# Performance work log

Hardware: AMD Instinct MI355X
Metric: run time of the kernel (lower is better)

Reference implementation:

```python
import jax, jax.numpy as jnp
import numpy as np

B = 128        # batch (images/texts)
N = 2048       # other texts per image
F_IMG = 1024   # raw image feature dim (abstracted encoder input)
F_TXT = 512    # raw text feature dim
D = 512        # embedding dim (num_features=512 in BasicNet)
TOPK = B - 1   # default topK = batch - 1


def setup_inputs() -> dict:
    key = jax.random.key(0)
    ks = jax.random.split(key, 6)
    return {
        "input_images": jax.random.normal(ks[0], (B, F_IMG), jnp.float32),
        "input_texts": jax.random.normal(ks[1], (B, F_TXT), jnp.float32),
        "other_texts": jax.random.normal(ks[2], (B, N, F_TXT), jnp.float32),
        "W_img": jax.random.normal(ks[3], (F_IMG, D), jnp.float32) / np.float32(np.sqrt(F_IMG)),
        "W_txt": jax.random.normal(ks[4], (F_TXT, D), jnp.float32) / np.float32(np.sqrt(F_TXT)),
        "logit_scale": jnp.asarray(np.log(1.0 / 0.07), jnp.float32),
    }


def reference(input_images, input_texts, other_texts, W_img, W_txt, logit_scale):
    K = TOPK
    # encoders abstracted as linear projections to D=512
    img = input_images @ W_img                                   # [B, D]
    img = img / jnp.linalg.norm(img, axis=1, keepdims=True)      # L2-normalize images
    txt = input_texts @ W_txt                                    # [B, D]
    txt = txt / jnp.linalg.norm(txt, axis=1, keepdims=True)      # row-wise norm == norm after concat
    oth = jnp.einsum('bnf,fd->bnd', other_texts, W_txt)          # [B, N, D]
    oth = oth / jnp.linalg.norm(oth, axis=2, keepdims=True)

    scale = jnp.exp(logit_scale)
    logit_in = scale * jnp.sum(img * txt, axis=1)                # [B] image_i . text_i
    logit_oth = scale * jnp.einsum('bd,bnd->bn', img, oth)       # [B, N]

    # descending sort + take top-K (lax.top_k returns sorted descending)
    topk_vals, _ = jax.lax.top_k(logit_oth, K)                   # [B, K]

    # indices = sorted(range(K) + [min(i, K-1)]): duplicate element p=min(i,K-1)
    rows = jnp.arange(B)
    cols = jnp.arange(K + 1)[None, :]                            # [1, K+1]
    p = jnp.minimum(rows, K - 1)[:, None]                        # [B, 1]
    gidx = jnp.where(cols <= p, cols, cols - 1)                  # [B, K+1]
    gathered = jnp.take_along_axis(topk_vals, gidx, axis=1)      # [B, K+1]

    # overwrite column i of row i with the positive (input text) logit
    out = jnp.where(cols == rows[:, None], logit_in[:, None], gathered)
    return out
```

## Files before the change

### kernel.cpp

```cpp
#include <hip/hip_runtime.h>
#include <hip/hip_bf16.h>
#include <math.h>

#define B_SZ 128
#define N_OTH 2048
#define F_IMG 1024
#define F_TXT 512
#define D_EMB 512
#define TOT (B_SZ * N_OTH)

typedef __attribute__((ext_vector_type(8))) short short8;
typedef __attribute__((ext_vector_type(16))) float f32x16;

static __device__ __forceinline__ ushort f2bf(float f) {
    __hip_bfloat16 h = __float2bfloat16(f);
    return *reinterpret_cast<ushort*>(&h);
}

static __device__ __forceinline__ void glds16(const float* g, float* l) {
    __builtin_amdgcn_global_load_lds((const __attribute__((address_space(1))) void*)g,
                                     (__attribute__((address_space(3))) void*)l, 16, 0, 0);
}

__global__ __launch_bounds__(512) void k_prep(const float* __restrict__ in_img,
                                              const float* __restrict__ in_txt,
                                              const float* __restrict__ W_img,
                                              const float* __restrict__ W_txt,
                                              const float* __restrict__ p_ls,
                                              float* __restrict__ img,
                                              float* __restrict__ logit_in,
                                              ushort* __restrict__ wf) {
    if (blockIdx.x >= B_SZ) {
        const int g = (blockIdx.x - B_SZ) * 512 + threadIdx.x;
        const int l = g & 63;
        const int frag = g >> 6;
        const int kstep = frag >> 4;
        const int ct = frag & 15;
        const int col = ct * 32 + (l & 31);
        const int kb = kstep * 16 + (l >> 5) * 8;
        short8 o;
#pragma unroll
        for (int j = 0; j < 8; ++j) o[j] = (short)f2bf(W_txt[(kb + j) * D_EMB + col]);
        *(short8*)(wf + (size_t)g * 8) = o;
        return;
    }
    const int b = blockIdx.x;
    const int d = threadIdx.x;
    __shared__ float row[F_IMG];
    __shared__ float wsum[8];
    __shared__ float s_rn;
    const int lane = d & 63, wv = d >> 6;

    for (int i = d; i < F_IMG; i += 512) row[i] = in_img[b * F_IMG + i];
    __syncthreads();
    float acc = 0.f;
#pragma unroll 8
    for (int f = 0; f < F_IMG; ++f) acc = fmaf(row[f], W_img[f * D_EMB + d], acc);
    float sq = acc * acc;
#pragma unroll
    for (int off = 32; off > 0; off >>= 1) sq += __shfl_down(sq, off);
    if (lane == 0) wsum[wv] = sq;
    __syncthreads();
    if (d == 0) {
        float s = 0.f;
        for (int w = 0; w < 8; ++w) s += wsum[w];
        s_rn = 1.0f / sqrtf(s);
    }
    __syncthreads();
    const float iv = acc * s_rn;
    img[b * D_EMB + d] = iv;

    __syncthreads();
    row[d] = in_txt[b * F_TXT + d];
    __syncthreads();
    float tacc = 0.f;
#pragma unroll 8
    for (int f = 0; f < F_TXT; ++f) tacc = fmaf(row[f], W_txt[f * D_EMB + d], tacc);
    float tsq = tacc * tacc;
#pragma unroll
    for (int off = 32; off > 0; off >>= 1) tsq += __shfl_down(tsq, off);
    __syncthreads();
    if (lane == 0) wsum[wv] = tsq;
    __syncthreads();
    if (d == 0) {
        float s = 0.f;
        for (int w = 0; w < 8; ++w) s += wsum[w];
        s_rn = 1.0f / sqrtf(s);
    }
    __syncthreads();
    float pd = (tacc * s_rn) * iv;
#pragma unroll
    for (int off = 32; off > 0; off >>= 1) pd += __shfl_down(pd, off);
    __syncthreads();
    if (lane == 0) wsum[wv] = pd;
    __syncthreads();
    if (d == 0) {
        float s = 0.f;
        for (int w = 0; w < 8; ++w) s += wsum[w];
        logit_in[b] = expf(p_ls[0]) * s;
    }
}

__global__ __launch_bounds__(256, 3) void k_gemm(const float* __restrict__ oth,
                                                 const ushort* __restrict__ wf,
                                                 const float* __restrict__ img,
                                                 float* __restrict__ numA,
                                                 float* __restrict__ denA) {
    __shared__ float sA[3][64 * 64];
    __shared__ float redN[4][64];
    __shared__ float redD[4][64];
    const int tid = threadIdx.x;
    const int l = tid & 63;
    const int wv = tid >> 6;
    const int strip = blockIdx.x >> 1;
    const int h = blockIdx.x & 1;
    const int b = strip >> 5;
    const size_t row0 = (size_t)strip * 64;

    const float* gA[4];
#pragma unroll
    for (int j = 0; j < 4; ++j) {
        const int row = wv * 16 + j * 4 + (l >> 4);
        const int gcol = (l & 15) ^ (row & 7);
        gA[j] = oth + (row0 + row) * F_TXT + gcol * 4;
    }

    const ushort* wbase = wf + ((size_t)(h * 8 + wv * 2) * 64 + l) * 8;

    f32x16 acc[2][2];
#pragma unroll
    for (int m = 0; m < 2; ++m)
#pragma unroll
        for (int n = 0; n < 2; ++n)
#pragma unroll
            for (int r = 0; r < 16; ++r) acc[m][n][r] = 0.f;

#pragma unroll
    for (int j = 0; j < 4; ++j) glds16(gA[j] + 0 * 64, &sA[0][(wv * 16 + j * 4) * 64]);
#pragma unroll
    for (int j = 0; j < 4; ++j) glds16(gA[j] + 1 * 64, &sA[1][(wv * 16 + j * 4) * 64]);
    __builtin_amdgcn_sched_barrier(0);
    asm volatile("s_waitcnt vmcnt(4)" ::: "memory");
    __builtin_amdgcn_sched_barrier(0);
    __builtin_amdgcn_s_barrier();
    __builtin_amdgcn_sched_barrier(0);

#pragma unroll
    for (int t = 0; t < 8; ++t) {
        const int cur = t % 3;
        short8 bfr[4][2];
#pragma unroll
        for (int ks = 0; ks < 4; ++ks)
#pragma unroll
            for (int n = 0; n < 2; ++n)
                bfr[ks][n] = *(const short8*)(wbase + (size_t)((t * 4 + ks) * 16 + n) * 512);
        __builtin_amdgcn_sched_barrier(0);
        if (t < 6) {
#pragma unroll
            for (int j = 0; j < 4; ++j)
                glds16(gA[j] + (t + 2) * 64, &sA[(t + 2) % 3][(wv * 16 + j * 4) * 64]);
        }
        __builtin_amdgcn_sched_barrier(0);
        __builtin_amdgcn_s_setprio(1);
#pragma unroll
        for (int ks = 0; ks < 4; ++ks) {
            short8 af[2];
#pragma unroll
            for (int m = 0; m < 2; ++m) {
                const int r = m * 32 + (l & 31);
                const int g0 = ks * 4 + (l >> 5) * 2;
                const float4 fa = *(const float4*)&sA[cur][r * 64 + ((g0 ^ (r & 7)) << 2)];
                const float4 fb = *(const float4*)&sA[cur][r * 64 + (((g0 + 1) ^ (r & 7)) << 2)];
                short8 v;
                v[0] = (short)f2bf(fa.x); v[1] = (short)f2bf(fa.y);
                v[2] = (short)f2bf(fa.z); v[3] = (short)f2bf(fa.w);
                v[4] = (short)f2bf(fb.x); v[5] = (short)f2bf(fb.y);
                v[6] = (short)f2bf(fb.z); v[7] = (short)f2bf(fb.w);
                af[m] = v;
            }
#pragma unroll
            for (int m = 0; m < 2; ++m)
#pragma unroll
                for (int n = 0; n < 2; ++n)
                    acc[m][n] = __builtin_amdgcn_mfma_f32_32x32x16_bf16(af[m], bfr[ks][n], acc[m][n], 0, 0, 0);
        }
        __builtin_amdgcn_s_setprio(0);
        if (t < 7) {
            asm volatile("s_waitcnt lgkmcnt(0)" ::: "memory");
            __builtin_amdgcn_sched_barrier(0);
            __builtin_amdgcn_s_barrier();
            __builtin_amdgcn_sched_barrier(0);
        }
    }

    float ic[2];
#pragma unroll
    for (int n = 0; n < 2; ++n)
        ic[n] = img[b * D_EMB + h * 256 + wv * 64 + n * 32 + (l & 31)];
#pragma unroll
    for (int m = 0; m < 2; ++m) {
#pragma unroll
        for (int rg = 0; rg < 16; ++rg) {
            const float p = acc[m][0][rg];
            const float q = acc[m][1][rg];
            float tn = p * ic[0] + q * ic[1];
            float td = p * p + q * q;
#pragma unroll
            for (int off = 1; off <= 16; off <<= 1) {
                tn += __shfl_xor(tn, off);
                td += __shfl_xor(td, off);
            }
            if ((l & 31) == 0) {
                const int r = m * 32 + (rg & 3) + 8 * (rg >> 2) + 4 * (l >> 5);
                redN[wv][r] = tn;
                redD[wv][r] = td;
            }
        }
    }
    __syncthreads();
    if (tid < 64) {
        float tn = 0.f, td = 0.f;
#pragma unroll
        for (int w = 0; w < 4; ++w) { tn += redN[w][tid]; td += redD[w][tid]; }
        numA[(size_t)h * TOT + row0 + tid] = tn;
        denA[(size_t)h * TOT + row0 + tid] = td;
    }
}

__global__ __launch_bounds__(512) void k_topk(const float* __restrict__ numA,
                                              const float* __restrict__ denA,
                                              const float* __restrict__ logit_in,
                                              const float* __restrict__ p_ls,
                                              float* __restrict__ out) {
    const int b = blockIdx.x;
    const int tid = threadIdx.x;
    const float scale = expf(p_ls[0]);
    __shared__ float a[N_OTH];
    for (int i = tid; i < N_OTH; i += 512) {
        const size_t idx = (size_t)b * N_OTH + i;
        const float nu = numA[idx] + numA[TOT + idx];
        const float de = denA[idx] + denA[TOT + idx];
        a[i] = scale * nu / sqrtf(de);
    }
    __syncthreads();
    for (unsigned k = 2; k <= N_OTH; k <<= 1) {
        for (unsigned j = k >> 1; j > 0; j >>= 1) {
#pragma unroll
            for (int s = 0; s < N_OTH / 512; ++s) {
                const unsigned i = tid + s * 512u;
                const unsigned ixj = i ^ j;
                if (ixj > i) {
                    const bool asc = ((i & k) == 0);
                    const float x = a[i], y = a[ixj];
                    if ((x > y) == asc) { a[i] = y; a[ixj] = x; }
                }
            }
            __syncthreads();
        }
    }
    if (tid < 128) {
        const int j = tid;
        float v;
        if (j == b) {
            v = logit_in[b];
        } else {
            const int m = j - (j > b ? 1 : 0);
            v = a[N_OTH - 1 - m];
        }
        out[b * 128 + j] = v;
    }
}

extern "C" void kernel_launch(void* const* d_in, const int* in_sizes, int n_in,
                              void* d_out, int out_size, void* d_ws, size_t ws_size,
                              hipStream_t stream) {
    const float* in_img = (const float*)d_in[0];
    const float* in_txt = (const float*)d_in[1];
    const float* oth    = (const float*)d_in[2];
    const float* W_img  = (const float*)d_in[3];
    const float* W_txt  = (const float*)d_in[4];
    const float* p_ls   = (const float*)d_in[5];
    float* out = (float*)d_out;

    float* ws = (float*)d_ws;
    float* img      = ws;
    float* logit_in = ws + 65536;
    float* numA     = ws + 65536 + 128;
    float* denA     = numA + 2 * TOT;
    ushort* wfrag   = (ushort*)(denA + 2 * TOT);

    k_prep<<<B_SZ + 64, 512, 0, stream>>>(in_img, in_txt, W_img, W_txt, p_ls, img, logit_in, wfrag);
    k_gemm<<<(TOT / 64) * 2, 256, 0, stream>>>(oth, wfrag, img, numA, denA);
    k_topk<<<B_SZ, 512, 0, stream>>>(numA, denA, logit_in, p_ls, out);
}
```

Baseline: 391.3 us.

## Switch GEMM staging to double-buffered LDS with 16-way swizzle and higher occupancy

Replaces the triple-buffered LDS pipeline (prefetch distance two, explicit vmcnt waits, sched barriers and setprio) with a simpler double buffer that prefetches one tile ahead and synchronises with __syncthreads. LDS per block drops from three 16KB tiles to two, and launch bounds rise from 3 to 4 blocks per CU to raise occupancy. The XOR swizzle changes from row&7 to row&15 using byte-offset addressing. The risk is less latency hiding per block, since the prefetch distance is shorter, and __syncthreads waits on all outstanding memory, which may serialise loads and compute.

```diff
diff --git a/kernel.cpp b/kernel.cpp
--- a/kernel.cpp
+++ b/kernel.cpp
@@ -101,12 +101,12 @@
     }
 }
 
-__global__ __launch_bounds__(256, 3) void k_gemm(const float* __restrict__ oth,
+__global__ __launch_bounds__(256, 4) void k_gemm(const float* __restrict__ oth,
                                                  const ushort* __restrict__ wf,
                                                  const float* __restrict__ img,
                                                  float* __restrict__ numA,
                                                  float* __restrict__ denA) {
-    __shared__ float sA[3][64 * 64];
+    __shared__ float sA[2][64 * 64];
     __shared__ float redN[4][64];
     __shared__ float redD[4][64];
     const int tid = threadIdx.x;
@@ -117,16 +117,23 @@
     const int b = strip >> 5;
     const size_t row0 = (size_t)strip * 64;
 
-    const float* gA[4];
+    const float* gsrc[4];
+    int ldsoff[4];
 #pragma unroll
     for (int j = 0; j < 4; ++j) {
-        const int row = wv * 16 + j * 4 + (l >> 4);
-        const int gcol = (l & 15) ^ (row & 7);
-        gA[j] = oth + (row0 + row) * F_TXT + gcol * 4;
+        const int r0 = wv * 16 + j * 4 + (l >> 4);
+        const int c = l & 15;
+        gsrc[j] = oth + (row0 + r0) * F_TXT + (size_t)((c ^ (r0 & 15)) * 4);
+        ldsoff[j] = (wv * 4 + j) * 256;
     }
 
     const ushort* wbase = wf + ((size_t)(h * 8 + wv * 2) * 64 + l) * 8;
 
+    const int rx = l & 15;
+    int rbase[2];
+#pragma unroll
+    for (int m = 0; m < 2; ++m) rbase[m] = (m * 32 + (l & 31)) * 256;
+
     f32x16 acc[2][2];
 #pragma unroll
     for (int m = 0; m < 2; ++m)
@@ -136,41 +143,31 @@
             for (int r = 0; r < 16; ++r) acc[m][n][r] = 0.f;
 
 #pragma unroll
-    for (int j = 0; j < 4; ++j) glds16(gA[j] + 0 * 64, &sA[0][(wv * 16 + j * 4) * 64]);
-#pragma unroll
-    for (int j = 0; j < 4; ++j) glds16(gA[j] + 1 * 64, &sA[1][(wv * 16 + j * 4) * 64]);
-    __builtin_amdgcn_sched_barrier(0);
-    asm volatile("s_waitcnt vmcnt(4)" ::: "memory");
-    __builtin_amdgcn_sched_barrier(0);
-    __builtin_amdgcn_s_barrier();
-    __builtin_amdgcn_sched_barrier(0);
+    for (int j = 0; j < 4; ++j) glds16(gsrc[j], &sA[0][0] + ldsoff[j]);
+    __syncthreads();
 
 #pragma unroll
     for (int t = 0; t < 8; ++t) {
-        const int cur = t % 3;
+        const int cur = t & 1;
+        if (t < 7) {
+#pragma unroll
+            for (int j = 0; j < 4; ++j)
+                glds16(gsrc[j] + (t + 1) * 64, &sA[cur ^ 1][0] + ldsoff[j]);
+        }
         short8 bfr[4][2];
 #pragma unroll
         for (int ks = 0; ks < 4; ++ks)
 #pragma unroll
             for (int n = 0; n < 2; ++n)
                 bfr[ks][n] = *(const short8*)(wbase + (size_t)((t * 4 + ks) * 16 + n) * 512);
-        __builtin_amdgcn_sched_barrier(0);
-        if (t < 6) {
-#pragma unroll
-            for (int j = 0; j < 4; ++j)
-                glds16(gA[j] + (t + 2) * 64, &sA[(t + 2) % 3][(wv * 16 + j * 4) * 64]);
-        }
-        __builtin_amdgcn_sched_barrier(0);
-        __builtin_amdgcn_s_setprio(1);
 #pragma unroll
         for (int ks = 0; ks < 4; ++ks) {
             short8 af[2];
 #pragma unroll
             for (int m = 0; m < 2; ++m) {
-                const int r = m * 32 + (l & 31);
                 const int g0 = ks * 4 + (l >> 5) * 2;
-                const float4 fa = *(const float4*)&sA[cur][r * 64 + ((g0 ^ (r & 7)) << 2)];
-                const float4 fb = *(const float4*)&sA[cur][r * 64 + (((g0 + 1) ^ (r & 7)) << 2)];
+                const float4 fa = *(const float4*)((const char*)&sA[cur][0] + rbase[m] + (((g0 + 0) ^ rx) << 4));
+                const float4 fb = *(const float4*)((const char*)&sA[cur][0] + rbase[m] + (((g0 + 1) ^ rx) << 4));
                 short8 v;
                 v[0] = (short)f2bf(fa.x); v[1] = (short)f2bf(fa.y);
                 v[2] = (short)f2bf(fa.z); v[3] = (short)f2bf(fa.w);
@@ -184,13 +181,7 @@
                 for (int n = 0; n < 2; ++n)
                     acc[m][n] = __builtin_amdgcn_mfma_f32_32x32x16_bf16(af[m], bfr[ks][n], acc[m][n], 0, 0, 0);
         }
-        __builtin_amdgcn_s_setprio(0);
-        if (t < 7) {
-            asm volatile("s_waitcnt lgkmcnt(0)" ::: "memory");
-            __builtin_amdgcn_sched_barrier(0);
-            __builtin_amdgcn_s_barrier();
-            __builtin_amdgcn_sched_barrier(0);
-        }
+        __syncthreads();
     }
 
     float ic[2];
@@ -201,10 +192,10 @@
     for (int m = 0; m < 2; ++m) {
 #pragma unroll
         for (int rg = 0; rg < 16; ++rg) {
-            const float p = acc[m][0][rg];
-            const float q = acc[m][1][rg];
-            float tn = p * ic[0] + q * ic[1];
-            float td = p * p + q * q;
+            const float pv = acc[m][0][rg];
+            const float qv = acc[m][1][rg];
+            float tn = pv * ic[0] + qv * ic[1];
+            float td = pv * pv + qv * qv;
 #pragma unroll
             for (int off = 1; off <= 16; off <<= 1) {
                 tn += __shfl_xor(tn, off);
```

After: 497.2 us. 1.27x slower.
